# Optimization experiments

Measured on AMD Instinct MI355X. Metric: run time of the kernel, lower is better.

## Reference

```python
import jax, jax.numpy as jnp
import numpy as np

SCALE = 16.0
TEMP = 0.07
EPS = 1e-8


def setup_inputs() -> dict:
    key = jax.random.key(0)
    k0, k1, k2, k3, k4 = jax.random.split(key, 5)
    B, D, h, w = 16, 128, 48, 48
    feats_a = jax.random.normal(k0, (B, D, h, w), jnp.float32)
    feats_b = jax.random.normal(k1, (B, D, h, w), jnp.float32)
    eye = jnp.eye(3, dtype=jnp.float32)
    # near-identity homographies (must be invertible)
    Hs_a = eye[None] + 0.02 * jax.random.normal(k2, (B, 3, 3), jnp.float32)
    Hs_b = eye[None] + 0.02 * jax.random.normal(k3, (B, 3, 3), jnp.float32)
    # near-identity affine with a small translation (in large-image pixels)
    M_a_b = jnp.array([[1.0, 0.0, 24.0], [0.0, 1.0, -16.0]], jnp.float32) \
        + 0.01 * jax.random.normal(k4, (2, 3), jnp.float32)
    return {"feats_a": feats_a, "feats_b": feats_b, "Hs_a": Hs_a, "Hs_b": Hs_b, "M_a_b": M_a_b}


def _transform_matrix(Hs_a, Hs_b, M_a_b):
    # Feat_A -> Img_A -> Large_A -> Large_B -> Img_B -> Feat_B
    B = Hs_a.shape[0]
    dt = Hs_a.dtype
    M3 = jnp.concatenate([M_a_b, jnp.array([[0.0, 0.0, 1.0]], dt)], axis=0)  # (3,3)
    S = jnp.diag(jnp.array([SCALE, SCALE, 1.0], dt))
    S_inv = jnp.diag(jnp.array([1.0 / SCALE, 1.0 / SCALE, 1.0], dt))
    Ha_inv = jnp.linalg.inv(Hs_a)  # (B,3,3)
    T = S_inv[None] @ Hs_b @ M3[None] @ Ha_inv @ S[None]
    return T


def _bilinear_sample(feats, grid):
    # feats (B,D,H,W); grid (B,h,w,2) normalized to [-1,1], align_corners=True,
    # zero padding for out-of-range samples (matches F.grid_sample).
    B, D, H, W = feats.shape
    h, w = grid.shape[1], grid.shape[2]
    ix = (grid[..., 0] + 1.0) * 0.5 * (W - 1)  # (B,h,w)
    iy = (grid[..., 1] + 1.0) * 0.5 * (H - 1)
    x0 = jnp.floor(ix); y0 = jnp.floor(iy)
    wx1 = ix - x0; wx0 = 1.0 - wx1
    wy1 = iy - y0; wy0 = 1.0 - wy1
    feats_flat = feats.reshape(B, D, H * W)

    def gather(xi, yi):
        valid = (xi >= 0) & (xi <= W - 1) & (yi >= 0) & (yi <= H - 1)
        xc = jnp.clip(xi, 0, W - 1).astype(jnp.int32)
        yc = jnp.clip(yi, 0, H - 1).astype(jnp.int32)
        idx = (yc * W + xc).reshape(B, -1)  # (B, h*w)
        v = jnp.take_along_axis(feats_flat, idx[:, None, :], axis=2)  # (B,D,h*w)
        return v * valid.reshape(B, 1, -1).astype(feats.dtype)

    out = (gather(x0, y0) * (wx0 * wy0).reshape(B, 1, -1)
           + gather(x0 + 1, y0) * (wx1 * wy0).reshape(B, 1, -1)
           + gather(x0, y0 + 1) * (wx0 * wy1).reshape(B, 1, -1)
           + gather(x0 + 1, y0 + 1) * (wx1 * wy1).reshape(B, 1, -1))
    return out.reshape(B, D, h, w)


def reference(feats_a, feats_b, Hs_a, Hs_b, M_a_b):
    B, D, h, w = feats_a.shape
    N = h * w
    H_b, W_b = feats_b.shape[2], feats_b.shape[3]
    T = _transform_matrix(Hs_a, Hs_b, M_a_b)  # (B,3,3)

    # homogeneous pixel grid of feats_a: (3, N)
    gy, gx = jnp.meshgrid(jnp.arange(h, dtype=jnp.float32), jnp.arange(w, dtype=jnp.float32), indexing='ij')
    coords = jnp.stack([gx.ravel(), gy.ravel(), jnp.ones(N, jnp.float32)], axis=0)  # (3,N)
    new = jnp.einsum('bij,jn->bin', T, coords)  # (B,3,N)
    z = new[:, 2, :] + EPS
    x_norm = 2.0 * (new[:, 0, :] / z) / (W_b - 1) - 1.0  # (B,N)
    y_norm = 2.0 * (new[:, 1, :] / z) / (H_b - 1) - 1.0
    grid = jnp.stack([x_norm, y_norm], axis=-1).reshape(B, h, w, 2)
    valid_mask = ((grid[..., 0] >= -1) & (grid[..., 0] <= 1)
                  & (grid[..., 1] >= -1) & (grid[..., 1] <= 1)).astype(jnp.float32)  # (B,h,w)

    warped_b = _bilinear_sample(feats_b, grid)  # (B,D,h,w)

    fa = feats_a.reshape(B, D, N).transpose(0, 2, 1)   # (B,N,D)
    wb = warped_b.reshape(B, D, N).transpose(0, 2, 1)  # (B,N,D)
    # F.normalize: x / max(||x||, eps) with eps=1e-12
    fa = fa / jnp.maximum(jnp.linalg.norm(fa, axis=2, keepdims=True), 1e-12)
    wb = wb / jnp.maximum(jnp.linalg.norm(wb, axis=2, keepdims=True), 1e-12)

    logits = jnp.einsum('bnd,bmd->bnm', fa, wb) / TEMP  # (B,N,N)
    # cross-entropy with labels = diagonal
    lse = jax.nn.logsumexp(logits, axis=-1)  # (B,N)
    diag = jnp.einsum('bnn->bn', logits)     # (B,N)
    loss_per = lse - diag                    # (B,N)

    mask = valid_mask.reshape(B, N)
    num_valid = mask.sum()
    total = (loss_per * mask).sum()
    return jnp.where(num_valid > 0, total / jnp.maximum(num_valid, 1.0), 0.0)
```

## Files before the change

### kernel.cpp

```cpp
#include <hip/hip_runtime.h>
#include <math.h>

#define B_ 16
#define D_ 128
#define HH 48
#define WW 48
#define N_ 2304
#define NC 72
#define SCALE_ 16.0f
#define INV_TEMP 14.285714285714286f
#define L2E_TEMP 20.60992915555662f
#define EPS_ 1e-8f
#define SPLITC 6
#define STAGES 6

typedef __attribute__((ext_vector_type(8))) short bf16x8;
typedef __attribute__((ext_vector_type(16))) float f32x16;

__device__ __forceinline__ short f2bf(float f) {
    union { float f; unsigned u; } v; v.f = f;
    unsigned r = v.u + 0x7FFFu + ((v.u >> 16) & 1u);
    return (short)(r >> 16);
}

__device__ __forceinline__ size_t frag_off(int b, int c, int ks, int lane) {
    return ((((size_t)b * NC + c) * 8 + ks) << 9) + (size_t)lane * 8;
}

__global__ __launch_bounds__(256) void k_prep(const float* __restrict__ fa,
                                              const float* __restrict__ fb,
                                              const float* __restrict__ Ha,
                                              const float* __restrict__ Hb,
                                              const float* __restrict__ Mab,
                                              float* __restrict__ maskA,
                                              short* __restrict__ faF,
                                              short* __restrict__ wbF) {
    __shared__ float part[4][2][32];
    const int b = blockIdx.y;
    const int rb = blockIdx.x;
    const int n0 = rb * 32;
    const int tid = threadIdx.x;
    const int lane = tid & 63, wv = tid >> 6;
    const int r = lane & 31, h = lane >> 5;
    const int n = n0 + r;

    float T[9];
    {
        const float* A = Ha + b * 9;
        const float* Bm = Hb + b * 9;
        float c00 = A[4] * A[8] - A[5] * A[7];
        float c01 = A[5] * A[6] - A[3] * A[8];
        float c02 = A[3] * A[7] - A[4] * A[6];
        float id = 1.f / (A[0] * c00 + A[1] * c01 + A[2] * c02);
        float inv[9] = { c00 * id, (A[2] * A[7] - A[1] * A[8]) * id, (A[1] * A[5] - A[2] * A[4]) * id,
                         c01 * id, (A[0] * A[8] - A[2] * A[6]) * id, (A[2] * A[3] - A[0] * A[5]) * id,
                         c02 * id, (A[1] * A[6] - A[0] * A[7]) * id, (A[0] * A[4] - A[1] * A[3]) * id };
        float M3[9] = {Mab[0], Mab[1], Mab[2], Mab[3], Mab[4], Mab[5], 0.f, 0.f, 1.f};
        float P1[9], P2[9];
        for (int i = 0; i < 3; ++i)
            for (int j = 0; j < 3; ++j) {
                float s = 0.f;
                for (int k = 0; k < 3; ++k) s += Bm[i * 3 + k] * M3[k * 3 + j];
                P1[i * 3 + j] = s;
            }
        for (int i = 0; i < 3; ++i)
            for (int j = 0; j < 3; ++j) {
                float s = 0.f;
                for (int k = 0; k < 3; ++k) s += P1[i * 3 + k] * inv[k * 3 + j];
                P2[i * 3 + j] = s;
            }
        const float sc[3] = {SCALE_, SCALE_, 1.f};
        for (int i = 0; i < 3; ++i)
            for (int j = 0; j < 3; ++j) T[i * 3 + j] = P2[i * 3 + j] * sc[j] / sc[i];
    }

    const float gx = (float)(n % WW), gy = (float)(n / WW);
    const float X = T[0] * gx + T[1] * gy + T[2];
    const float Y = T[3] * gx + T[4] * gy + T[5];
    const float z = T[6] * gx + T[7] * gy + T[8] + EPS_;
    const float xn = 2.f * (X / z) / (float)(WW - 1) - 1.f;
    const float yn = 2.f * (Y / z) / (float)(HH - 1) - 1.f;
    const float msk = (xn >= -1.f && xn <= 1.f && yn >= -1.f && yn <= 1.f) ? 1.f : 0.f;
    const float ix = (xn + 1.f) * 0.5f * (float)(WW - 1);
    const float iy = (yn + 1.f) * 0.5f * (float)(HH - 1);
    const float x0f = floorf(ix), y0f = floorf(iy);
    const float wx1 = ix - x0f, wx0 = 1.f - wx1;
    const float wy1 = iy - y0f, wy0 = 1.f - wy1;
    const bool vx0 = (x0f >= 0.f) && (x0f <= 47.f);
    const bool vx1 = (x0f + 1.f >= 0.f) && (x0f + 1.f <= 47.f);
    const bool vy0 = (y0f >= 0.f) && (y0f <= 47.f);
    const bool vy1 = (y0f + 1.f >= 0.f) && (y0f + 1.f <= 47.f);
    const float w00 = (vx0 && vy0) ? wx0 * wy0 : 0.f;
    const float w01 = (vx1 && vy0) ? wx1 * wy0 : 0.f;
    const float w10 = (vx0 && vy1) ? wx0 * wy1 : 0.f;
    const float w11 = (vx1 && vy1) ? wx1 * wy1 : 0.f;
    const int x0c = (int)fminf(fmaxf(x0f, 0.f), 47.f);
    const int x1c = (int)fminf(fmaxf(x0f + 1.f, 0.f), 47.f);
    const int y0c = (int)fminf(fmaxf(y0f, 0.f), 47.f);
    const int y1c = (int)fminf(fmaxf(y0f + 1.f, 0.f), 47.f);
    const int o00 = y0c * WW + x0c, o01 = y0c * WW + x1c;
    const int o10 = y1c * WW + x0c, o11 = y1c * WW + x1c;

    const float* fab = fa + (size_t)b * D_ * N_;
    const float* fbb = fb + (size_t)b * D_ * N_;

    float av[2][8], wvv[2][8];
    float sA = 0.f, sW = 0.f;
    #pragma unroll
    for (int g = 0; g < 2; ++g) {
        const int ks = wv + 4 * g;
        const int dbase = ks * 16 + h * 8;
        #pragma unroll
        for (int j = 0; j < 8; ++j) {
            const int d = dbase + j;
            const float* p = fbb + (size_t)d * N_;
            float w = w00 * p[o00] + w01 * p[o01] + w10 * p[o10] + w11 * p[o11];
            float a = fab[(size_t)d * N_ + n];
            av[g][j] = a; wvv[g][j] = w;
            sA += a * a; sW += w * w;
        }
    }
    sA += __shfl_xor(sA, 32);
    sW += __shfl_xor(sW, 32);
    if (lane < 32) { part[wv][0][r] = sA; part[wv][1][r] = sW; }
    if (tid < 32) maskA[b * N_ + n0 + r] = msk;
    __syncthreads();
    const float rnA = 1.f / fmaxf(sqrtf(part[0][0][r] + part[1][0][r] + part[2][0][r] + part[3][0][r]), 1e-12f);
    const float rnW = 1.f / fmaxf(sqrtf(part[0][1][r] + part[1][1][r] + part[2][1][r] + part[3][1][r]), 1e-12f);

    #pragma unroll
    for (int g = 0; g < 2; ++g) {
        const int ks = wv + 4 * g;
        bf16x8 oa, ow;
        #pragma unroll
        for (int j = 0; j < 8; ++j) {
            oa[j] = f2bf(av[g][j] * rnA);
            ow[j] = f2bf(wvv[g][j] * rnW);
        }
        size_t off = frag_off(b, rb, ks, lane);
        *(bf16x8*)(faF + off) = oa;
        *(bf16x8*)(wbF + off) = ow;
    }
}

__global__ __launch_bounds__(256, 4) void k_loss(const short* __restrict__ faF,
                                                 const short* __restrict__ wbF,
                                                 float* __restrict__ Zpart,
                                                 float* __restrict__ dgbuf) {
    __shared__ short bbuf[2][8192];
    __shared__ float s_Z[128];
    const int bx = blockIdx.x;
    const int cs = blockIdx.y;
    const int b = blockIdx.z;
    const int tid = threadIdx.x;
    const int lane = tid & 63, w = tid >> 6;
    const int l31 = lane & 31, h = lane >> 5;
    const int rc = bx * 4 + w;

    bf16x8 af[8];
    #pragma unroll
    for (int ks = 0; ks < 8; ++ks)
        af[ks] = *(const bf16x8*)(faF + frag_off(b, rc, ks, lane));

    float Z[16];
    #pragma unroll
    for (int i = 0; i < 16; ++i) Z[i] = 0.f;

    const short* bsrc = wbF + frag_off(b, cs * 12, 0, 0);

    #pragma unroll
    for (int i = 0; i < 4; ++i)
        *(float4*)(&bbuf[0][tid * 8 + i * 2048]) = *(const float4*)(bsrc + tid * 8 + i * 2048);
    __syncthreads();

    for (int s = 0; s < STAGES; ++s) {
        float4 pf[4];
        const bool more = (s + 1 < STAGES);
        if (more) {
            const short* src = bsrc + (s + 1) * 8192;
            #pragma unroll
            for (int i = 0; i < 4; ++i) pf[i] = *(const float4*)(src + tid * 8 + i * 2048);
        }
        const short* bb = &bbuf[s & 1][0];
        f32x16 C0, C1;
        #pragma unroll
        for (int i = 0; i < 16; ++i) { C0[i] = 0.f; C1[i] = 0.f; }
        #pragma unroll
        for (int ks = 0; ks < 8; ++ks) {
            bf16x8 b0 = *(const bf16x8*)(bb + ks * 512 + lane * 8);
            bf16x8 b1 = *(const bf16x8*)(bb + 4096 + ks * 512 + lane * 8);
            C0 = __builtin_amdgcn_mfma_f32_32x32x16_bf16(af[ks], b0, C0, 0, 0, 0);
            C1 = __builtin_amdgcn_mfma_f32_32x32x16_bf16(af[ks], b1, C1, 0, 0, 0);
        }
        #pragma unroll
        for (int i = 0; i < 16; ++i) {
            Z[i] += exp2f(fmaf(C0[i], L2E_TEMP, -L2E_TEMP))
                  + exp2f(fmaf(C1[i], L2E_TEMP, -L2E_TEMP));
        }
        const int jc0 = cs * 12 + 2 * s, jc1 = jc0 + 1;
        if (jc0 == rc) {
            #pragma unroll
            for (int i = 0; i < 16; ++i) {
                int rr = (i & 3) + 8 * (i >> 2) + 4 * h;
                if (l31 == rr) dgbuf[b * N_ + rc * 32 + rr] = INV_TEMP * C0[i];
            }
        }
        if (jc1 == rc) {
            #pragma unroll
            for (int i = 0; i < 16; ++i) {
                int rr = (i & 3) + 8 * (i >> 2) + 4 * h;
                if (l31 == rr) dgbuf[b * N_ + rc * 32 + rr] = INV_TEMP * C1[i];
            }
        }
        if (more) {
            short* dst = &bbuf[(s + 1) & 1][0];
            #pragma unroll
            for (int i = 0; i < 4; ++i) *(float4*)(dst + tid * 8 + i * 2048) = pf[i];
        }
        __syncthreads();
    }

    #pragma unroll
    for (int i = 0; i < 16; ++i) {
        float z = Z[i];
        z += __shfl_xor(z, 1);
        z += __shfl_xor(z, 2);
        z += __shfl_xor(z, 4);
        z += __shfl_xor(z, 8);
        z += __shfl_xor(z, 16);
        if (l31 == 0) {
            int rr = (i & 3) + 8 * (i >> 2) + 4 * h;
            s_Z[w * 32 + rr] = z;
        }
    }
    __syncthreads();
    if (tid < 128)
        Zpart[((size_t)cs * B_ + b) * N_ + bx * 128 + tid] = s_Z[tid];
}

__global__ __launch_bounds__(256) void k_pass2(const float* __restrict__ maskA,
                                               const float* __restrict__ Zpart,
                                               const float* __restrict__ dgbuf,
                                               float* __restrict__ partials) {
    const int idx = blockIdx.x * 256 + threadIdx.x;
    float Zs = 0.f;
    #pragma unroll
    for (int s = 0; s < SPLITC; ++s) Zs += Zpart[(size_t)s * B_ * N_ + idx];
    const float m = maskA[idx];
    float lossv = (logf(Zs) + INV_TEMP - dgbuf[idx]) * m;
    float cm = m;
    for (int off = 1; off < 64; off <<= 1) {
        lossv += __shfl_xor(lossv, off);
        cm += __shfl_xor(cm, off);
    }
    __shared__ float s[8];
    const int wv = threadIdx.x >> 6;
    if ((threadIdx.x & 63) == 0) { s[wv * 2] = lossv; s[wv * 2 + 1] = cm; }
    __syncthreads();
    if (threadIdx.x == 0) {
        partials[blockIdx.x * 2] = s[0] + s[2] + s[4] + s[6];
        partials[blockIdx.x * 2 + 1] = s[1] + s[3] + s[5] + s[7];
    }
}

__global__ void k_final(const float* __restrict__ partials, float* __restrict__ out) {
    const int t = threadIdx.x;
    float tt = 0.f, cc = 0.f;
    for (int i = t; i < 144; i += 64) { tt += partials[i * 2]; cc += partials[i * 2 + 1]; }
    for (int off = 1; off < 64; off <<= 1) {
        tt += __shfl_xor(tt, off);
        cc += __shfl_xor(cc, off);
    }
    if (t == 0) out[0] = (cc > 0.f) ? tt / fmaxf(cc, 1.f) : 0.f;
}

extern "C" void kernel_launch(void* const* d_in, const int* in_sizes, int n_in,
                              void* d_out, int out_size, void* d_ws, size_t ws_size,
                              hipStream_t stream) {
    const float* fa = (const float*)d_in[0];
    const float* fb = (const float*)d_in[1];
    const float* Ha = (const float*)d_in[2];
    const float* Hb = (const float*)d_in[3];
    const float* M = (const float*)d_in[4];
    float* out = (float*)d_out;

    float* wsf = (float*)d_ws;
    float* Zpart = wsf;
    float* dgbuf = Zpart + (size_t)SPLITC * B_ * N_;
    float* maskA = dgbuf + B_ * N_;
    float* partials = maskA + B_ * N_;
    short* faF = (short*)(partials + 512);
    short* wbF = faF + (size_t)B_ * NC * 8 * 512;

    hipLaunchKernelGGL(k_prep, dim3(NC, B_), dim3(256), 0, stream,
                       fa, fb, Ha, Hb, M, maskA, faF, wbF);
    hipLaunchKernelGGL(k_loss, dim3(N_ / 128, SPLITC, B_), dim3(256), 0, stream,
                       faF, wbF, Zpart, dgbuf);
    hipLaunchKernelGGL(k_pass2, dim3(B_ * N_ / 256), dim3(256), 0, stream,
                       maskA, Zpart, dgbuf, partials);
    hipLaunchKernelGGL(k_final, dim3(1), dim3(64), 0, stream, partials, out);
}
```

Before: 138.1 us.

## Load B fragments straight to registers and give each wave two row tiles

The loss kernel drops the shared-memory double buffer and its block barriers. Each wave now loads the B fragments directly from global memory into registers with a two-deep software prefetch, and each wave handles two 32-row A tiles so every B fragment feeds two MFMAs. The column split doubles to 12 chunks of 6 and the row blocks halve, which keeps the total block count the same. Register pressure rises (launch bounds drop to 2) and B is read from global by every wave rather than once per block through LDS.

```diff
diff --git a/kernel.cpp b/kernel.cpp
--- a/kernel.cpp
+++ b/kernel.cpp
@@ -11,8 +11,8 @@
 #define INV_TEMP 14.285714285714286f
 #define L2E_TEMP 20.60992915555662f
 #define EPS_ 1e-8f
-#define SPLITC 6
-#define STAGES 6
+#define SPLITC 12
+#define CCHUNK 6
 
 typedef __attribute__((ext_vector_type(8))) short bf16x8;
 typedef __attribute__((ext_vector_type(16))) float f32x16;
@@ -143,99 +143,101 @@
     }
 }
 
-__global__ __launch_bounds__(256, 4) void k_loss(const short* __restrict__ faF,
+__global__ __launch_bounds__(256, 2) void k_loss(const short* __restrict__ faF,
                                                  const short* __restrict__ wbF,
                                                  float* __restrict__ Zpart,
                                                  float* __restrict__ dgbuf) {
-    __shared__ short bbuf[2][8192];
-    __shared__ float s_Z[128];
     const int bx = blockIdx.x;
     const int cs = blockIdx.y;
     const int b = blockIdx.z;
     const int tid = threadIdx.x;
     const int lane = tid & 63, w = tid >> 6;
     const int l31 = lane & 31, h = lane >> 5;
-    const int rc = bx * 4 + w;
-
-    bf16x8 af[8];
-    #pragma unroll
-    for (int ks = 0; ks < 8; ++ks)
-        af[ks] = *(const bf16x8*)(faF + frag_off(b, rc, ks, lane));
-
-    float Z[16];
-    #pragma unroll
-    for (int i = 0; i < 16; ++i) Z[i] = 0.f;
-
-    const short* bsrc = wbF + frag_off(b, cs * 12, 0, 0);
-
-    #pragma unroll
-    for (int i = 0; i < 4; ++i)
-        *(float4*)(&bbuf[0][tid * 8 + i * 2048]) = *(const float4*)(bsrc + tid * 8 + i * 2048);
-    __syncthreads();
-
-    for (int s = 0; s < STAGES; ++s) {
-        float4 pf[4];
-        const bool more = (s + 1 < STAGES);
-        if (more) {
-            const short* src = bsrc + (s + 1) * 8192;
-            #pragma unroll
-            for (int i = 0; i < 4; ++i) pf[i] = *(const float4*)(src + tid * 8 + i * 2048);
-        }
-        const short* bb = &bbuf[s & 1][0];
+    const int rc0 = bx * 8 + w * 2;
+    const int rc1 = rc0 + 1;
+
+    bf16x8 a0[8], a1[8];
+    #pragma unroll
+    for (int ks = 0; ks < 8; ++ks) {
+        a0[ks] = *(const bf16x8*)(faF + frag_off(b, rc0, ks, lane));
+        a1[ks] = *(const bf16x8*)(faF + frag_off(b, rc1, ks, lane));
+    }
+
+    float Z0[16], Z1[16];
+    #pragma unroll
+    for (int i = 0; i < 16; ++i) { Z0[i] = 0.f; Z1[i] = 0.f; }
+
+    const int c0 = cs * CCHUNK;
+    const short* bbase = wbF + frag_off(b, c0, 0, lane);
+
+    auto process = [&](const bf16x8* bf, int cj) {
         f32x16 C0, C1;
         #pragma unroll
         for (int i = 0; i < 16; ++i) { C0[i] = 0.f; C1[i] = 0.f; }
         #pragma unroll
         for (int ks = 0; ks < 8; ++ks) {
-            bf16x8 b0 = *(const bf16x8*)(bb + ks * 512 + lane * 8);
-            bf16x8 b1 = *(const bf16x8*)(bb + 4096 + ks * 512 + lane * 8);
-            C0 = __builtin_amdgcn_mfma_f32_32x32x16_bf16(af[ks], b0, C0, 0, 0, 0);
-            C1 = __builtin_amdgcn_mfma_f32_32x32x16_bf16(af[ks], b1, C1, 0, 0, 0);
+            C0 = __builtin_amdgcn_mfma_f32_32x32x16_bf16(a0[ks], bf[ks], C0, 0, 0, 0);
+            C1 = __builtin_amdgcn_mfma_f32_32x32x16_bf16(a1[ks], bf[ks], C1, 0, 0, 0);
         }
         #pragma unroll
         for (int i = 0; i < 16; ++i) {
-            Z[i] += exp2f(fmaf(C0[i], L2E_TEMP, -L2E_TEMP))
-                  + exp2f(fmaf(C1[i], L2E_TEMP, -L2E_TEMP));
-        }
-        const int jc0 = cs * 12 + 2 * s, jc1 = jc0 + 1;
-        if (jc0 == rc) {
+            Z0[i] += exp2f(fmaf(C0[i], L2E_TEMP, -L2E_TEMP));
+            Z1[i] += exp2f(fmaf(C1[i], L2E_TEMP, -L2E_TEMP));
+        }
+        if (cj == rc0) {
             #pragma unroll
             for (int i = 0; i < 16; ++i) {
                 int rr = (i & 3) + 8 * (i >> 2) + 4 * h;
-                if (l31 == rr) dgbuf[b * N_ + rc * 32 + rr] = INV_TEMP * C0[i];
+                if (l31 == rr) dgbuf[b * N_ + rc0 * 32 + rr] = INV_TEMP * C0[i];
             }
         }
-        if (jc1 == rc) {
+        if (cj == rc1) {
             #pragma unroll
             for (int i = 0; i < 16; ++i) {
                 int rr = (i & 3) + 8 * (i >> 2) + 4 * h;
-                if (l31 == rr) dgbuf[b * N_ + rc * 32 + rr] = INV_TEMP * C1[i];
+                if (l31 == rr) dgbuf[b * N_ + rc1 * 32 + rr] = INV_TEMP * C1[i];
             }
         }
-        if (more) {
-            short* dst = &bbuf[(s + 1) & 1][0];
+    };
+
+    bf16x8 bfA[8], bfB[8];
+    #pragma unroll
+    for (int ks = 0; ks < 8; ++ks)
+        bfA[ks] = *(const bf16x8*)(bbase + (ks << 9));
+
+    #pragma unroll
+    for (int jp = 0; jp < CCHUNK; jp += 2) {
+        {
+            const short* s1 = bbase + (size_t)(jp + 1) * 4096;
             #pragma unroll
-            for (int i = 0; i < 4; ++i) *(float4*)(dst + tid * 8 + i * 2048) = pf[i];
-        }
-        __syncthreads();
-    }
-
+            for (int ks = 0; ks < 8; ++ks)
+                bfB[ks] = *(const bf16x8*)(s1 + (ks << 9));
+        }
+        process(bfA, c0 + jp);
+        if (jp + 2 < CCHUNK) {
+            const short* s2 = bbase + (size_t)(jp + 2) * 4096;
+            #pragma unroll
+            for (int ks = 0; ks < 8; ++ks)
+                bfA[ks] = *(const bf16x8*)(s2 + (ks << 9));
+        }
+        process(bfB, c0 + jp + 1);
+    }
+
+    float* zp = Zpart + ((size_t)cs * B_ + b) * N_;
     #pragma unroll
     for (int i = 0; i < 16; ++i) {
-        float z = Z[i];
-        z += __shfl_xor(z, 1);
-        z += __shfl_xor(z, 2);
-        z += __shfl_xor(z, 4);
-        z += __shfl_xor(z, 8);
-        z += __shfl_xor(z, 16);
+        float z0 = Z0[i], z1 = Z1[i];
+        #pragma unroll
+        for (int off = 1; off < 32; off <<= 1) {
+            z0 += __shfl_xor(z0, off);
+            z1 += __shfl_xor(z1, off);
+        }
         if (l31 == 0) {
-            int rr = (i & 3) + 8 * (i >> 2) + 4 * h;
-            s_Z[w * 32 + rr] = z;
-        }
-    }
-    __syncthreads();
-    if (tid < 128)
-        Zpart[((size_t)cs * B_ + b) * N_ + bx * 128 + tid] = s_Z[tid];
+            const int rr = (i & 3) + 8 * (i >> 2) + 4 * h;
+            zp[rc0 * 32 + rr] = z0;
+            zp[rc1 * 32 + rr] = z1;
+        }
+    }
 }
 
 __global__ __launch_bounds__(256) void k_pass2(const float* __restrict__ maskA,
@@ -294,7 +296,7 @@
 
     hipLaunchKernelGGL(k_prep, dim3(NC, B_), dim3(256), 0, stream,
                        fa, fb, Ha, Hb, M, maskA, faF, wbF);
-    hipLaunchKernelGGL(k_loss, dim3(N_ / 128, SPLITC, B_), dim3(256), 0, stream,
+    hipLaunchKernelGGL(k_loss, dim3(N_ / 256, SPLITC, B_), dim3(256), 0, stream,
                        faF, wbF, Zpart, dgbuf);
     hipLaunchKernelGGL(k_pass2, dim3(B_ * N_ / 256), dim3(256), 0, stream,
                        maskA, Zpart, dgbuf, partials);
```

New measurement: 179.0 us. 29.6% more time.

## Use direct global-to-LDS loads and XCD-aware block remapping in loss kernel

Applied to the files above, without the earlier changes.

The B-tile staging in the loss kernel now uses global_load_lds to write straight into shared memory. This replaces the register round-trip through float4 prefetch and LDS store. The 3D grid is also flattened into a 1D grid, and blocks are remapped so each XCD handles two batches, which should improve L2 reuse of the wbF and faF data. This relies on the async LDS load completing before the __syncthreads barrier, and on correct wait semantics.

```diff
diff --git a/kernel.cpp b/kernel.cpp
--- a/kernel.cpp
+++ b/kernel.cpp
@@ -25,6 +25,12 @@
 
 __device__ __forceinline__ size_t frag_off(int b, int c, int ks, int lane) {
     return ((((size_t)b * NC + c) * 8 + ks) << 9) + (size_t)lane * 8;
+}
+
+__device__ __forceinline__ void gld16(const short* g, short* l) {
+    __builtin_amdgcn_global_load_lds(
+        (const __attribute__((address_space(1))) void*)g,
+        (__attribute__((address_space(3))) void*)l, 16, 0, 0);
 }
 
 __global__ __launch_bounds__(256) void k_prep(const float* __restrict__ fa,
@@ -149,9 +155,13 @@
                                                  float* __restrict__ dgbuf) {
     __shared__ short bbuf[2][8192];
     __shared__ float s_Z[128];
-    const int bx = blockIdx.x;
-    const int cs = blockIdx.y;
-    const int b = blockIdx.z;
+    const int lin = blockIdx.x;
+    const int xcd = lin & 7;
+    const int i0 = lin >> 3;
+    const int b = xcd * 2 + (i0 / 108);
+    const int r108 = i0 % 108;
+    const int bx = r108 % 18;
+    const int cs = r108 / 18;
     const int tid = threadIdx.x;
     const int lane = tid & 63, w = tid >> 6;
     const int l31 = lane & 31, h = lane >> 5;
@@ -168,19 +178,18 @@
 
     const short* bsrc = wbF + frag_off(b, cs * 12, 0, 0);
 
-    #pragma unroll
-    for (int i = 0; i < 4; ++i)
-        *(float4*)(&bbuf[0][tid * 8 + i * 2048]) = *(const float4*)(bsrc + tid * 8 + i * 2048);
+    #define STAGE_B(nb, s) { \
+        const short* sg = bsrc + (size_t)(s) * 8192 + w * 2048 + lane * 8; \
+        short* sl = &bbuf[nb][w * 2048]; \
+        _Pragma("unroll") \
+        for (int j = 0; j < 4; ++j) gld16(sg + j * 512, sl + j * 512); \
+    }
+
+    STAGE_B(0, 0);
     __syncthreads();
 
     for (int s = 0; s < STAGES; ++s) {
-        float4 pf[4];
-        const bool more = (s + 1 < STAGES);
-        if (more) {
-            const short* src = bsrc + (s + 1) * 8192;
-            #pragma unroll
-            for (int i = 0; i < 4; ++i) pf[i] = *(const float4*)(src + tid * 8 + i * 2048);
-        }
+        if (s + 1 < STAGES) STAGE_B((s + 1) & 1, s + 1);
         const short* bb = &bbuf[s & 1][0];
         f32x16 C0, C1;
         #pragma unroll
@@ -212,13 +221,9 @@
                 if (l31 == rr) dgbuf[b * N_ + rc * 32 + rr] = INV_TEMP * C1[i];
             }
         }
-        if (more) {
-            short* dst = &bbuf[(s + 1) & 1][0];
-            #pragma unroll
-            for (int i = 0; i < 4; ++i) *(float4*)(dst + tid * 8 + i * 2048) = pf[i];
-        }
         __syncthreads();
     }
+    #undef STAGE_B
 
     #pragma unroll
     for (int i = 0; i < 16; ++i) {
@@ -294,7 +299,7 @@
 
     hipLaunchKernelGGL(k_prep, dim3(NC, B_), dim3(256), 0, stream,
                        fa, fb, Ha, Hb, M, maskA, faF, wbF);
-    hipLaunchKernelGGL(k_loss, dim3(N_ / 128, SPLITC, B_), dim3(256), 0, stream,
+    hipLaunchKernelGGL(k_loss, dim3(8 * 216), dim3(256), 0, stream,
                        faF, wbF, Zpart, dgbuf);
     hipLaunchKernelGGL(k_pass2, dim3(B_ * N_ / 256), dim3(256), 0, stream,
                        maskA, Zpart, dgbuf, partials);
```

Measured after the change: 138.0 us. Within noise of the previous version (-0.1%).
